# Performance work log

Hardware: AMD Instinct MI355X
Metric: run time of the kernel (lower is better)

The kernel has to match this reference:

```python
import jax, jax.numpy as jnp
import numpy as np

B_SZ, SEQ, D_IN, D_ST, D_OUT = 16, 8192, 128, 128, 128


def setup_inputs() -> dict:
    key = jax.random.key(0)
    ku, ka, kb, kc, kd = jax.random.split(key, 5)
    u = jax.random.normal(ku, (B_SZ, SEQ, D_IN), dtype=jnp.float32)
    # A scaled to spectral radius ~0.9 so the long recurrence stays stable
    A = jax.random.normal(ka, (D_ST, D_ST), dtype=jnp.float32) * (0.9 / np.sqrt(D_ST))
    B = jax.random.normal(kb, (D_ST, D_IN), dtype=jnp.float32) * (1.0 / np.sqrt(D_IN))
    C = jax.random.normal(kc, (D_OUT, D_ST), dtype=jnp.float32) * (1.0 / np.sqrt(D_ST))
    D = jax.random.normal(kd, (D_OUT, D_IN), dtype=jnp.float32) * (1.0 / np.sqrt(D_IN))
    return {"u": u, "A": A, "B": B, "C": C, "D": D}


def reference(u, A, B, C, D):
    # x_t = x_{t-1} A^T + u_t B^T ; y_t = x_t C^T + u_t D^T ; x_0 = 0
    batch = u.shape[0]
    state0 = jnp.zeros((batch, A.shape[0]), dtype=u.dtype)

    def step(state, u_t):  # state: [B, S_dim], u_t: [B, D_in]
        new_state = state @ A.T + u_t @ B.T
        y = new_state @ C.T + u_t @ D.T
        return new_state, y

    u_t_first = jnp.swapaxes(u, 0, 1)  # [SEQ, B, D_in]
    _, ys = jax.lax.scan(step, state0, u_t_first)
    return jnp.swapaxes(ys, 0, 1)  # [B, SEQ, D_out]
```

## Files before the change

kernel.cpp:

```cpp
#include <hip/hip_runtime.h>


#define SEQ 8192
#define DD  128
#define WIN 16

typedef __bf16 bf16t;
typedef __bf16 bf16x8 __attribute__((ext_vector_type(8)));
typedef float  f32x4  __attribute__((ext_vector_type(4)));

#define MFMA(a,b,c) __builtin_amdgcn_mfma_f32_16x16x32_bf16(a,b,c,0,0,0)

__device__ __forceinline__ int swc(int r, int c) {
    int g = c >> 3;
    g = (g & ~7) | ((g ^ r) & 7);
    return (g << 3) | (c & 7);
}
__device__ __forceinline__ bf16x8 lds_frag(const bf16t* T, int stride, int row, int col) {
    return *(const bf16x8*)(T + row * stride + swc(row, col));
}
__device__ __forceinline__ bf16x8 cvt8(float4 a, float4 b) {
    bf16x8 r;
    r[0]=(bf16t)a.x; r[1]=(bf16t)a.y; r[2]=(bf16t)a.z; r[3]=(bf16t)a.w;
    r[4]=(bf16t)b.x; r[5]=(bf16t)b.y; r[6]=(bf16t)b.z; r[7]=(bf16t)b.w;
    return r;
}
__device__ __forceinline__ bf16x8 bzero8() {
    bf16x8 z;
#pragma unroll
    for (int e = 0; e < 8; e++) z[e] = (bf16t)0.f;
    return z;
}
__device__ __forceinline__ f32x4 fzero4() { f32x4 z = {0.f, 0.f, 0.f, 0.f}; return z; }

__global__ __launch_bounds__(512, 2) void k_squares(const float* __restrict__ A,
                                                    float* __restrict__ Sq,
                                                    float* __restrict__ Iden,
                                                    bf16t* __restrict__ E1pad) {
    int tid = threadIdx.x, lane = tid & 63, wid = tid >> 6;
    if (blockIdx.x == 1) {
        for (int i = tid; i < 16384; i += 512)
            Iden[i] = ((i >> 7) == (i & 127)) ? 1.f : 0.f;
        bf16x8 z = bzero8();
        for (int i = tid; i < WIN * 16 * 128 / 8; i += 512)
            *(bf16x8*)(E1pad + i * 8) = z;
        return;
    }
    __shared__ bf16t H0[128*128], T0[128*128], H1[128*128], T1[128*128];
    {
        int r = tid >> 2, c0 = (tid & 3) * 32;
#pragma unroll
        for (int e = 0; e < 4; e++) {
            float4 va = *(const float4*)(A + r*128 + c0 + e*8);
            float4 vb = *(const float4*)(A + r*128 + c0 + e*8 + 4);
            bf16x8 h = cvt8(va, vb);
            *(bf16x8*)(H0 + r*128 + swc(r, c0 + e*8)) = h;
#pragma unroll
            for (int x = 0; x < 8; x++) {
                int cc = c0 + e*8 + x;
                T0[cc*128 + swc(cc, r)] = h[x];
            }
        }
    }
    __syncthreads();
    bf16t *cH = H0, *cT = T0, *nH = H1, *nT = T1;
    for (int lvl = 0; lvl < 6; lvl++) {
        f32x4 acc[8];
#pragma unroll
        for (int nf = 0; nf < 8; nf++) acc[nf] = fzero4();
        int m = 16*wid + (lane & 15);
#pragma unroll
        for (int q = 0; q < 4; q++) {
            bf16x8 af = lds_frag(cH, 128, m, q*32 + ((lane >> 4) << 3));
#pragma unroll
            for (int nf = 0; nf < 8; nf++) {
                bf16x8 bv = lds_frag(cT, 128, nf*16 + (lane & 15), q*32 + ((lane >> 4) << 3));
                acc[nf] = MFMA(af, bv, acc[nf]);
            }
        }
#pragma unroll
        for (int nf = 0; nf < 8; nf++)
#pragma unroll
            for (int rr = 0; rr < 4; rr++) {
                int row = 16*wid + ((lane >> 4) << 2) + rr;
                int col = nf*16 + (lane & 15);
                float v = acc[nf][rr];
                bf16t hv = (bf16t)v;
                nH[row*128 + swc(row, col)] = hv;
                nT[col*128 + swc(col, row)] = hv;
                Sq[lvl*16384 + row*128 + col] = v;
            }
        __syncthreads();
        bf16t* t;
        t = cH; cH = nH; nH = t;
        t = cT; cT = nT; nT = t;
    }
}

__global__ __launch_bounds__(512) void k_mats(const float* __restrict__ A,
                                              const float* __restrict__ B,
                                              const float* __restrict__ C,
                                              const float* __restrict__ Dm,
                                              const float* __restrict__ Sq,
                                              const float* __restrict__ Iden,
                                              bf16t* __restrict__ KbigT,
                                              bf16t* __restrict__ DistT,
                                              bf16t* __restrict__ WdT,
                                              bf16t* __restrict__ QT) {
    __shared__ bf16t Hc[128*128], Hn[128*128], Tg[128*128];
    int tid = threadIdx.x, lane = tid & 63, wid = tid >> 6;
    int bid = blockIdx.x;
    const float* G[10] = {A, B, C, Sq, Sq + 16384, Sq + 2*16384,
                          Sq + 3*16384, Sq + 4*16384, Sq + 5*16384, Iden};
    int ch[6]; int nc = 0;
    bf16t* dst = nullptr; long dstride = 128;
    bool plusD = false;
    if (bid < 8) {
        int d = bid;
        if (d & 4) ch[nc++] = 4;
        if (d & 2) ch[nc++] = 3;
        if (d & 1) ch[nc++] = 0;
        ch[nc++] = 1;
        if (nc == 1) ch[nc++] = 9;
        dst = KbigT + (7 - d) * 128; dstride = 1024;
    } else if (bid < 24) {
        int e = bid - 8;
        if (e & 8) ch[nc++] = 8;
        if (e & 4) ch[nc++] = 7;
        if (e & 2) ch[nc++] = 6;
        if (e & 1) ch[nc++] = 5;
        if (nc == 0) ch[nc++] = 9;
        if (nc == 1) ch[nc++] = 9;
        dst = DistT + e * 16384;
    } else if (bid < 32) {
        int d = bid - 24;
        ch[nc++] = 2;
        if (d & 4) ch[nc++] = 4;
        if (d & 2) ch[nc++] = 3;
        if (d & 1) ch[nc++] = 0;
        ch[nc++] = 1;
        plusD = (d == 0);
        dst = WdT + d * 16384;
    } else {
        int k = bid - 32 + 1;
        ch[nc++] = 2;
        if (k & 8) ch[nc++] = 5;
        if (k & 4) ch[nc++] = 4;
        if (k & 2) ch[nc++] = 3;
        if (k & 1) ch[nc++] = 0;
        dst = QT + (k - 1) * 16384;
    }
    {
        const float* g0 = G[ch[0]];
        int r = tid >> 2, c0 = (tid & 3) * 32;
#pragma unroll
        for (int e = 0; e < 4; e++) {
            float4 va = *(const float4*)(g0 + r*128 + c0 + e*8);
            float4 vb = *(const float4*)(g0 + r*128 + c0 + e*8 + 4);
            *(bf16x8*)(Hc + r*128 + swc(r, c0 + e*8)) = cvt8(va, vb);
        }
    }
    f32x4 acc[8];
    bf16t* cur = Hc; bf16t* nxt = Hn;
    for (int i = 1; i < nc; i++) {
        const float* g = G[ch[i]];
        __syncthreads();
        {
            int r = tid >> 2, c0 = (tid & 3) * 32;
#pragma unroll
            for (int e = 0; e < 4; e++) {
                float4 va = *(const float4*)(g + r*128 + c0 + e*8);
                float4 vb = *(const float4*)(g + r*128 + c0 + e*8 + 4);
                bf16x8 h = cvt8(va, vb);
#pragma unroll
                for (int x = 0; x < 8; x++) {
                    int cc = c0 + e*8 + x;
                    Tg[cc*128 + swc(cc, r)] = h[x];
                }
            }
        }
        __syncthreads();
#pragma unroll
        for (int nf = 0; nf < 8; nf++) acc[nf] = fzero4();
        int m = 16*wid + (lane & 15);
#pragma unroll
        for (int q = 0; q < 4; q++) {
            bf16x8 af = lds_frag(cur, 128, m, q*32 + ((lane >> 4) << 3));
#pragma unroll
            for (int nf = 0; nf < 8; nf++) {
                bf16x8 bv = lds_frag(Tg, 128, nf*16 + (lane & 15), q*32 + ((lane >> 4) << 3));
                acc[nf] = MFMA(af, bv, acc[nf]);
            }
        }
        if (i + 1 < nc) {
#pragma unroll
            for (int nf = 0; nf < 8; nf++)
#pragma unroll
                for (int rr = 0; rr < 4; rr++) {
                    int row = 16*wid + ((lane >> 4) << 2) + rr;
                    int col = nf*16 + (lane & 15);
                    nxt[row*128 + swc(row, col)] = (bf16t)acc[nf][rr];
                }
            bf16t* t = cur; cur = nxt; nxt = t;
        }
    }
#pragma unroll
    for (int nf = 0; nf < 8; nf++)
#pragma unroll
        for (int rr = 0; rr < 4; rr++) {
            int row = 16*wid + ((lane >> 4) << 2) + rr;
            int col = nf*16 + (lane & 15);
            float v = acc[nf][rr];
            if (plusD) v += Dm[row*128 + col];
            dst[(long)row * dstride + col] = (bf16t)v;
        }
}

__device__ __forceinline__ void stage_u2(const float* __restrict__ u, int c0,
                                         bf16t* __restrict__ U, int tid) {
    int row = tid >> 4;
    int cl = row >> 4, b = row & 15;
    const float* up = u + (long)b * SEQ * DD + (long)(c0 + cl) * 1024 + (tid & 15) * 8;
#pragma unroll
    for (int e = 0; e < 8; e++) {
        int col = (tid & 15) * 8 + e * 128;
        float4 v0 = *(const float4*)(up + e * 128);
        float4 v1 = *(const float4*)(up + e * 128 + 4);
        *(bf16x8*)(U + row * 1024 + swc(row, col)) = cvt8(v0, v1);
    }
}

__global__ __launch_bounds__(512, 2) void k_pass1(const float* __restrict__ u,
                                                  const bf16t* __restrict__ KbigT,
                                                  bf16t* __restrict__ E1pad) {
    __shared__ bf16t U[32*1024];
    int tid = threadIdx.x, lane = tid & 63, w = tid >> 6;
    int c0 = blockIdx.x * 2;
    int n = (w << 4) + (lane & 15), kg = lane >> 4;
    stage_u2(u, c0, U, tid);
    __syncthreads();
    f32x4 acc[2][2];
#pragma unroll
    for (int m = 0; m < 2; m++) { acc[m][0] = fzero4(); acc[m][1] = fzero4(); }
#pragma unroll
    for (int s = 0; s < 32; s++) {
        bf16x8 bk = *(const bf16x8*)(KbigT + n*1024 + s*32 + kg*8);
#pragma unroll
        for (int m = 0; m < 2; m++) {
            bf16x8 af = lds_frag(U, 1024, m*16 + (lane & 15), s*32 + kg*8);
            acc[m][s & 1] = MFMA(af, bk, acc[m][s & 1]);
        }
    }
#pragma unroll
    for (int m = 0; m < 2; m++) {
        f32x4 a = acc[m][0] + acc[m][1];
#pragma unroll
        for (int rr = 0; rr < 4; rr++) {
            int b = (kg << 2) + rr;
            E1pad[((long)(WIN + c0 + m)*16 + b)*128 + n] = (bf16t)a[rr];
        }
    }
}

__global__ __launch_bounds__(512, 2) void k_passE(const bf16t* __restrict__ E1pad,
                                                  const bf16t* __restrict__ DistT,
                                                  bf16t* __restrict__ Xent) {
    __shared__ bf16t Et[272*128];
    int tid = threadIdx.x, lane = tid & 63, w = tid >> 6;
    int c0 = blockIdx.x * 2;
    int n = (w << 4) + (lane & 15), kg = lane >> 4;
    {
        const bf16t* src = E1pad + (long)c0*16*128;
        for (int idx = tid; idx < 272*16; idx += 512) {
            int row = idx >> 4, gc = (idx & 15) * 8;
            bf16x8 v = *(const bf16x8*)(src + row*128 + gc);
            *(bf16x8*)(Et + row*128 + swc(row, gc)) = v;
        }
    }
    __syncthreads();
    f32x4 acc[2][2];
#pragma unroll
    for (int m = 0; m < 2; m++) { acc[m][0] = fzero4(); acc[m][1] = fzero4(); }
#pragma unroll
    for (int j = 1; j <= WIN; j++) {
#pragma unroll
        for (int kk = 0; kk < 4; kk++) {
            bf16x8 bf = *(const bf16x8*)(DistT + (long)(j-1)*16384 + n*128 + kk*32 + kg*8);
#pragma unroll
            for (int m = 0; m < 2; m++) {
                bf16x8 af = lds_frag(Et, 128, (m + WIN - j)*16 + (lane & 15), kk*32 + kg*8);
                acc[m][j & 1] = MFMA(af, bf, acc[m][j & 1]);
            }
        }
    }
#pragma unroll
    for (int m = 0; m < 2; m++) {
        f32x4 a = acc[m][0] + acc[m][1];
#pragma unroll
        for (int rr = 0; rr < 4; rr++) {
            int b = (kg << 2) + rr;
            Xent[((long)(c0 + m)*16 + b)*128 + n] = (bf16t)a[rr];
        }
    }
}

__global__ __launch_bounds__(512, 2) void k_pass2(const float* __restrict__ u,
                                                  const bf16t* __restrict__ Xent,
                                                  const bf16t* __restrict__ WdT,
                                                  const bf16t* __restrict__ QT,
                                                  float* __restrict__ out) {
    __shared__ bf16t U[32*1024];
    __shared__ bf16t X[32*128];
    int tid = threadIdx.x, lane = tid & 63, w = tid >> 6;
    int c0 = blockIdx.x * 2;
    int n = (w << 4) + (lane & 15), kg = lane >> 4;
    bf16x8 bc[2][4];
#pragma unroll
    for (int d = 0; d < 2; d++)
#pragma unroll
        for (int k4 = 0; k4 < 4; k4++)
            bc[d][k4] = *(const bf16x8*)(WdT + (long)d*16384 + n*128 + k4*32 + kg*8);
    stage_u2(u, c0, U, tid);
    {
        const bf16t* xs = Xent + (long)c0*16*128;
        int row = tid >> 4, gc = (tid & 15) * 8;
        bf16x8 v = *(const bf16x8*)(xs + row*128 + gc);
        *(bf16x8*)(X + row*128 + swc(row, gc)) = v;
    }
    __syncthreads();
    f32x4 acc[2][8];
#pragma unroll
    for (int m = 0; m < 2; m++)
#pragma unroll
        for (int t = 0; t < 8; t++) acc[m][t] = fzero4();
#pragma unroll
    for (int p = 0; p < 8; p++) {
#pragma unroll
        for (int k4 = 0; k4 < 4; k4++) {
            int s = p*4 + k4;
            bf16x8 af0 = lds_frag(U, 1024, (lane & 15),      s*32 + kg*8);
            bf16x8 af1 = lds_frag(U, 1024, 16 + (lane & 15), s*32 + kg*8);
#pragma unroll
            for (int t = p; t < 8; t++) {
                int d = t - p;
                bf16x8 bf = (d < 2) ? bc[d][k4]
                    : *(const bf16x8*)(WdT + (long)d*16384 + n*128 + k4*32 + kg*8);
                acc[0][t] = MFMA(af0, bf, acc[0][t]);
                acc[1][t] = MFMA(af1, bf, acc[1][t]);
            }
        }
    }
#pragma unroll
    for (int k4 = 0; k4 < 4; k4++) {
        bf16x8 af0 = lds_frag(X, 128, (lane & 15),      k4*32 + kg*8);
        bf16x8 af1 = lds_frag(X, 128, 16 + (lane & 15), k4*32 + kg*8);
#pragma unroll
        for (int t = 0; t < 8; t++) {
            bf16x8 bf = *(const bf16x8*)(QT + (long)t*16384 + n*128 + k4*32 + kg*8);
            acc[0][t] = MFMA(af0, bf, acc[0][t]);
            acc[1][t] = MFMA(af1, bf, acc[1][t]);
        }
    }
#pragma unroll
    for (int m = 0; m < 2; m++)
#pragma unroll
        for (int t = 0; t < 8; t++)
#pragma unroll
            for (int rr = 0; rr < 4; rr++) {
                int b = (kg << 2) + rr;
                out[(long)b*SEQ*DD + ((long)(c0 + m)*8 + t)*DD + n] = acc[m][t][rr];
            }
}

extern "C" void kernel_launch(void* const* d_in, const int* in_sizes, int n_in,
                              void* d_out, int out_size, void* d_ws, size_t ws_size,
                              hipStream_t stream) {
    (void)in_sizes; (void)n_in; (void)out_size; (void)ws_size;
    const float* u = (const float*)d_in[0];
    const float* A = (const float*)d_in[1];
    const float* B = (const float*)d_in[2];
    const float* C = (const float*)d_in[3];
    const float* D = (const float*)d_in[4];
    float* out = (float*)d_out;
    float* Sq    = (float*)d_ws;
    float* Iden  = Sq + 6*16384;
    bf16t* KbigT = (bf16t*)(Iden + 16384);
    bf16t* DistT = KbigT + 131072;
    bf16t* WdT   = DistT + 16*16384;
    bf16t* QT    = WdT + 8*16384;
    bf16t* E1pad = QT + 8*16384;
    bf16t* Xent  = E1pad + (long)(WIN + 1024)*2048;

    k_squares<<<2,  512, 0, stream>>>(A, Sq, Iden, E1pad);
    k_mats  <<<40,  512, 0, stream>>>(A, B, C, D, Sq, Iden, KbigT, DistT, WdT, QT);
    k_pass1 <<<512, 512, 0, stream>>>(u, KbigT, E1pad);
    k_passE <<<512, 512, 0, stream>>>(E1pad, DistT, Xent);
    k_pass2 <<<512, 512, 0, stream>>>(u, Xent, WdT, QT, out);
}
```

Measured before the change: 144.7 us.

## Fuse chunk-entry state pass into output pass, one chunk per block

Removes the separate k_passE kernel and its Xent round trip. k_pass2 now computes each chunk's entry state itself from E1pad and DistT, reading global memory directly, and writes the result into LDS. Blocks now own one 8-step chunk instead of two, so grids double to 1024 and LDS per block is halved. A strided chunk_of mapping spreads neighbouring chunks across blocks. The cost is that MFMA B-operand reuse across two chunks is lost, so weight fragments are reloaded from global/L2 twice as often, and the removed register caching of WdT means more global loads.

```diff
diff --git a/kernel.cpp b/kernel.cpp
--- a/kernel.cpp
+++ b/kernel.cpp
@@ -32,6 +32,18 @@
     return z;
 }
 __device__ __forceinline__ f32x4 fzero4() { f32x4 z = {0.f, 0.f, 0.f, 0.f}; return z; }
+
+__device__ __forceinline__ void stage_u1(const float* __restrict__ u, int c0,
+                                         bf16t* __restrict__ U, int tid) {
+    int row = tid >> 5, cb = (tid & 31) * 8;
+    const float* up = u + (long)row * SEQ * DD + (long)c0 * 1024 + cb;
+#pragma unroll
+    for (int e = 0; e < 4; e++) {
+        float4 v0 = *(const float4*)(up + e * 256);
+        float4 v1 = *(const float4*)(up + e * 256 + 4);
+        *(bf16x8*)(U + row * 1024 + swc(row, cb + e * 256)) = cvt8(v0, v1);
+    }
+}
 
 __global__ __launch_bounds__(512, 2) void k_squares(const float* __restrict__ A,
                                                     float* __restrict__ Sq,
@@ -216,160 +228,98 @@
         }
 }
 
-__device__ __forceinline__ void stage_u2(const float* __restrict__ u, int c0,
-                                         bf16t* __restrict__ U, int tid) {
-    int row = tid >> 4;
-    int cl = row >> 4, b = row & 15;
-    const float* up = u + (long)b * SEQ * DD + (long)(c0 + cl) * 1024 + (tid & 15) * 8;
-#pragma unroll
-    for (int e = 0; e < 8; e++) {
-        int col = (tid & 15) * 8 + e * 128;
-        float4 v0 = *(const float4*)(up + e * 128);
-        float4 v1 = *(const float4*)(up + e * 128 + 4);
-        *(bf16x8*)(U + row * 1024 + swc(row, col)) = cvt8(v0, v1);
-    }
-}
-
-__global__ __launch_bounds__(512, 2) void k_pass1(const float* __restrict__ u,
-                                                  const bf16t* __restrict__ KbigT,
-                                                  bf16t* __restrict__ E1pad) {
-    __shared__ bf16t U[32*1024];
+__device__ __forceinline__ int chunk_of(int bid) {
+    return (bid & 7) * 128 + (bid >> 3);
+}
+
+__global__ __launch_bounds__(512) void k_pass1(const float* __restrict__ u,
+                                               const bf16t* __restrict__ KbigT,
+                                               bf16t* __restrict__ E1pad) {
+    __shared__ bf16t U[16*1024];
     int tid = threadIdx.x, lane = tid & 63, w = tid >> 6;
-    int c0 = blockIdx.x * 2;
+    int c0 = chunk_of(blockIdx.x);
     int n = (w << 4) + (lane & 15), kg = lane >> 4;
-    stage_u2(u, c0, U, tid);
+    stage_u1(u, c0, U, tid);
     __syncthreads();
-    f32x4 acc[2][2];
-#pragma unroll
-    for (int m = 0; m < 2; m++) { acc[m][0] = fzero4(); acc[m][1] = fzero4(); }
+    f32x4 a0 = fzero4(), a1 = fzero4();
 #pragma unroll
     for (int s = 0; s < 32; s++) {
         bf16x8 bk = *(const bf16x8*)(KbigT + n*1024 + s*32 + kg*8);
-#pragma unroll
-        for (int m = 0; m < 2; m++) {
-            bf16x8 af = lds_frag(U, 1024, m*16 + (lane & 15), s*32 + kg*8);
-            acc[m][s & 1] = MFMA(af, bk, acc[m][s & 1]);
-        }
-    }
-#pragma unroll
-    for (int m = 0; m < 2; m++) {
-        f32x4 a = acc[m][0] + acc[m][1];
+        bf16x8 af = lds_frag(U, 1024, lane & 15, s*32 + kg*8);
+        if (s & 1) a1 = MFMA(af, bk, a1);
+        else       a0 = MFMA(af, bk, a0);
+    }
+    f32x4 a = a0 + a1;
+#pragma unroll
+    for (int rr = 0; rr < 4; rr++)
+        E1pad[((long)(WIN + c0)*16 + kg*4 + rr)*128 + n] = (bf16t)a[rr];
+}
+
+__global__ __launch_bounds__(512) void k_pass2(const float* __restrict__ u,
+                                               const bf16t* __restrict__ E1pad,
+                                               const bf16t* __restrict__ DistT,
+                                               const bf16t* __restrict__ WdT,
+                                               const bf16t* __restrict__ QT,
+                                               float* __restrict__ out) {
+    __shared__ bf16t U[16*1024];
+    __shared__ bf16t X[16*128];
+    int tid = threadIdx.x, lane = tid & 63, w = tid >> 6;
+    int c0 = chunk_of(blockIdx.x);
+    int n = (w << 4) + (lane & 15), kg = lane >> 4;
+    stage_u1(u, c0, U, tid);
+    {
+        f32x4 x0 = fzero4(), x1 = fzero4();
+#pragma unroll
+        for (int j = 1; j <= WIN; j++) {
+            const bf16t* ea = E1pad + ((long)(c0 + WIN - j)*16 + (lane & 15))*128;
+            const bf16t* db = DistT + (long)(j-1)*16384 + n*128;
+#pragma unroll
+            for (int kk = 0; kk < 4; kk++) {
+                bf16x8 af = *(const bf16x8*)(ea + kk*32 + kg*8);
+                bf16x8 bf = *(const bf16x8*)(db + kk*32 + kg*8);
+                if (j & 1) x1 = MFMA(af, bf, x1);
+                else       x0 = MFMA(af, bf, x0);
+            }
+        }
+        f32x4 xs = x0 + x1;
 #pragma unroll
         for (int rr = 0; rr < 4; rr++) {
-            int b = (kg << 2) + rr;
-            E1pad[((long)(WIN + c0 + m)*16 + b)*128 + n] = (bf16t)a[rr];
-        }
-    }
-}
-
-__global__ __launch_bounds__(512, 2) void k_passE(const bf16t* __restrict__ E1pad,
-                                                  const bf16t* __restrict__ DistT,
-                                                  bf16t* __restrict__ Xent) {
-    __shared__ bf16t Et[272*128];
-    int tid = threadIdx.x, lane = tid & 63, w = tid >> 6;
-    int c0 = blockIdx.x * 2;
-    int n = (w << 4) + (lane & 15), kg = lane >> 4;
-    {
-        const bf16t* src = E1pad + (long)c0*16*128;
-        for (int idx = tid; idx < 272*16; idx += 512) {
-            int row = idx >> 4, gc = (idx & 15) * 8;
-            bf16x8 v = *(const bf16x8*)(src + row*128 + gc);
-            *(bf16x8*)(Et + row*128 + swc(row, gc)) = v;
+            int xr = kg*4 + rr;
+            X[xr*128 + swc(xr, n)] = (bf16t)xs[rr];
         }
     }
     __syncthreads();
-    f32x4 acc[2][2];
-#pragma unroll
-    for (int m = 0; m < 2; m++) { acc[m][0] = fzero4(); acc[m][1] = fzero4(); }
-#pragma unroll
-    for (int j = 1; j <= WIN; j++) {
-#pragma unroll
-        for (int kk = 0; kk < 4; kk++) {
-            bf16x8 bf = *(const bf16x8*)(DistT + (long)(j-1)*16384 + n*128 + kk*32 + kg*8);
-#pragma unroll
-            for (int m = 0; m < 2; m++) {
-                bf16x8 af = lds_frag(Et, 128, (m + WIN - j)*16 + (lane & 15), kk*32 + kg*8);
-                acc[m][j & 1] = MFMA(af, bf, acc[m][j & 1]);
-            }
-        }
-    }
-#pragma unroll
-    for (int m = 0; m < 2; m++) {
-        f32x4 a = acc[m][0] + acc[m][1];
-#pragma unroll
-        for (int rr = 0; rr < 4; rr++) {
-            int b = (kg << 2) + rr;
-            Xent[((long)(c0 + m)*16 + b)*128 + n] = (bf16t)a[rr];
-        }
-    }
-}
-
-__global__ __launch_bounds__(512, 2) void k_pass2(const float* __restrict__ u,
-                                                  const bf16t* __restrict__ Xent,
-                                                  const bf16t* __restrict__ WdT,
-                                                  const bf16t* __restrict__ QT,
-                                                  float* __restrict__ out) {
-    __shared__ bf16t U[32*1024];
-    __shared__ bf16t X[32*128];
-    int tid = threadIdx.x, lane = tid & 63, w = tid >> 6;
-    int c0 = blockIdx.x * 2;
-    int n = (w << 4) + (lane & 15), kg = lane >> 4;
-    bf16x8 bc[2][4];
-#pragma unroll
-    for (int d = 0; d < 2; d++)
-#pragma unroll
-        for (int k4 = 0; k4 < 4; k4++)
-            bc[d][k4] = *(const bf16x8*)(WdT + (long)d*16384 + n*128 + k4*32 + kg*8);
-    stage_u2(u, c0, U, tid);
-    {
-        const bf16t* xs = Xent + (long)c0*16*128;
-        int row = tid >> 4, gc = (tid & 15) * 8;
-        bf16x8 v = *(const bf16x8*)(xs + row*128 + gc);
-        *(bf16x8*)(X + row*128 + swc(row, gc)) = v;
-    }
-    __syncthreads();
-    f32x4 acc[2][8];
-#pragma unroll
-    for (int m = 0; m < 2; m++)
-#pragma unroll
-        for (int t = 0; t < 8; t++) acc[m][t] = fzero4();
+    f32x4 acc[8];
+#pragma unroll
+    for (int t = 0; t < 8; t++) acc[t] = fzero4();
 #pragma unroll
     for (int p = 0; p < 8; p++) {
 #pragma unroll
         for (int k4 = 0; k4 < 4; k4++) {
-            int s = p*4 + k4;
-            bf16x8 af0 = lds_frag(U, 1024, (lane & 15),      s*32 + kg*8);
-            bf16x8 af1 = lds_frag(U, 1024, 16 + (lane & 15), s*32 + kg*8);
+            bf16x8 af = lds_frag(U, 1024, lane & 15, (p*4 + k4)*32 + kg*8);
 #pragma unroll
             for (int t = p; t < 8; t++) {
-                int d = t - p;
-                bf16x8 bf = (d < 2) ? bc[d][k4]
-                    : *(const bf16x8*)(WdT + (long)d*16384 + n*128 + k4*32 + kg*8);
-                acc[0][t] = MFMA(af0, bf, acc[0][t]);
-                acc[1][t] = MFMA(af1, bf, acc[1][t]);
+                bf16x8 bf = *(const bf16x8*)(WdT + (long)(t - p)*16384 + n*128 + k4*32 + kg*8);
+                acc[t] = MFMA(af, bf, acc[t]);
             }
         }
     }
 #pragma unroll
     for (int k4 = 0; k4 < 4; k4++) {
-        bf16x8 af0 = lds_frag(X, 128, (lane & 15),      k4*32 + kg*8);
-        bf16x8 af1 = lds_frag(X, 128, 16 + (lane & 15), k4*32 + kg*8);
+        bf16x8 af = lds_frag(X, 128, lane & 15, k4*32 + kg*8);
 #pragma unroll
         for (int t = 0; t < 8; t++) {
             bf16x8 bf = *(const bf16x8*)(QT + (long)t*16384 + n*128 + k4*32 + kg*8);
-            acc[0][t] = MFMA(af0, bf, acc[0][t]);
-            acc[1][t] = MFMA(af1, bf, acc[1][t]);
-        }
-    }
-#pragma unroll
-    for (int m = 0; m < 2; m++)
-#pragma unroll
-        for (int t = 0; t < 8; t++)
-#pragma unroll
-            for (int rr = 0; rr < 4; rr++) {
-                int b = (kg << 2) + rr;
-                out[(long)b*SEQ*DD + ((long)(c0 + m)*8 + t)*DD + n] = acc[m][t][rr];
-            }
+            acc[t] = MFMA(af, bf, acc[t]);
+        }
+    }
+#pragma unroll
+    for (int t = 0; t < 8; t++)
+#pragma unroll
+        for (int rr = 0; rr < 4; rr++) {
+            int b = kg*4 + rr;
+            out[(long)b*SEQ*DD + ((long)c0*8 + t)*DD + n] = acc[t][rr];
+        }
 }
 
 extern "C" void kernel_launch(void* const* d_in, const int* in_sizes, int n_in,
@@ -389,11 +339,9 @@
     bf16t* WdT   = DistT + 16*16384;
     bf16t* QT    = WdT + 8*16384;
     bf16t* E1pad = QT + 8*16384;
-    bf16t* Xent  = E1pad + (long)(WIN + 1024)*2048;
-
-    k_squares<<<2,  512, 0, stream>>>(A, Sq, Iden, E1pad);
-    k_mats  <<<40,  512, 0, stream>>>(A, B, C, D, Sq, Iden, KbigT, DistT, WdT, QT);
-    k_pass1 <<<512, 512, 0, stream>>>(u, KbigT, E1pad);
-    k_passE <<<512, 512, 0, stream>>>(E1pad, DistT, Xent);
-    k_pass2 <<<512, 512, 0, stream>>>(u, Xent, WdT, QT, out);
-}
+
+    k_squares<<<2,   512, 0, stream>>>(A, Sq, Iden, E1pad);
+    k_mats   <<<40,  512, 0, stream>>>(A, B, C, D, Sq, Iden, KbigT, DistT, WdT, QT);
+    k_pass1  <<<1024, 512, 0, stream>>>(u, KbigT, E1pad);
+    k_pass2  <<<1024, 512, 0, stream>>>(u, E1pad, DistT, WdT, QT, out);
+}
```

Result: slower. 254.9 us (+76.1%).
